# Kernel optimization log

Measured on AMD Instinct MI355X. Metric: run time of the kernel, lower is better.

The kernel has to match this reference:

```python
import jax, jax.numpy as jnp
import numpy as np

DIM_MODEL = 1024
NUM_HEADS = 16
DIM_HEAD = 64
B, S = 2, 2048


def setup_inputs() -> dict:
    key = jax.random.key(0)
    ks = jax.random.split(key, 10)
    scale = 1.0 / np.sqrt(DIM_MODEL)
    inp = {
        "x": jax.random.normal(ks[0], (B, S, DIM_MODEL), dtype=jnp.float32),
        "padding_mask": jax.random.randint(ks[1], (B, S), 0, 2, dtype=jnp.int32),
        "Wq": jax.random.normal(ks[2], (DIM_MODEL, DIM_MODEL), dtype=jnp.float32) * scale,
        "bq": jnp.zeros((DIM_MODEL,), dtype=jnp.float32),
        "Wk": jax.random.normal(ks[3], (DIM_MODEL, DIM_MODEL), dtype=jnp.float32) * scale,
        "bk": jnp.zeros((DIM_MODEL,), dtype=jnp.float32),
        "Wv": jax.random.normal(ks[4], (DIM_MODEL, DIM_MODEL), dtype=jnp.float32) * scale,
        "bv": jnp.zeros((DIM_MODEL,), dtype=jnp.float32),
        "Wo": jax.random.normal(ks[5], (DIM_MODEL, DIM_MODEL), dtype=jnp.float32) * scale,
        "bo": jnp.zeros((DIM_MODEL,), dtype=jnp.float32),
    }
    return inp


def reference(x, padding_mask, Wq, bq, Wk, bk, Wv, bv, Wo, bo):
    b, s, _ = x.shape
    dot_scale = jnp.sqrt(jnp.asarray(DIM_HEAD, dtype=x.dtype))
    # projections -> (b, h, s, d)
    q = (x @ Wq + bq).reshape(b, s, NUM_HEADS, DIM_HEAD).transpose(0, 2, 1, 3)
    k = (x @ Wk + bk).reshape(b, s, NUM_HEADS, DIM_HEAD).transpose(0, 2, 1, 3)
    v = (x @ Wv + bv).reshape(b, s, NUM_HEADS, DIM_HEAD).transpose(0, 2, 1, 3)
    # scores (b, h, s, s)
    scores = jnp.einsum("bhqd,bhkd->bhqk", q, k) / dot_scale
    mask = (padding_mask == 1)[:, None, None, :]  # (b,1,1,s) over key positions
    scores = jnp.where(mask, -jnp.inf, scores)
    attn = jax.nn.softmax(scores, axis=-1)
    out = jnp.einsum("bhqk,bhkd->bhqd", attn, v)
    out = out.transpose(0, 2, 1, 3).reshape(b, s, NUM_HEADS * DIM_HEAD)
    return out @ Wo + bo
```

## Files before the change

kernel.cpp:

```cpp
#include <hip/hip_runtime.h>
#include <hip/hip_bf16.h>
#include <stdint.h>
#include <math.h>

#define D_MODEL 1024
#define NHEAD   16
#define DHEAD   64
#define BATCH   2
#define SEQ     2048
#define M_TOK   (BATCH * SEQ)

#define QSCALE 0.18033688011112042f

typedef __attribute__((ext_vector_type(8))) short   short8;
typedef __attribute__((ext_vector_type(8))) __bf16  bf16x8;
typedef __attribute__((ext_vector_type(4))) float   f32x4;

__device__ inline short f2bf(float f) {
  unsigned int u = __builtin_bit_cast(unsigned int, f);
  unsigned int r = (u + 0x7FFFu + ((u >> 16) & 1u)) >> 16;
  return (short)(unsigned short)r;
}
__device__ inline short f2bf_fast(float f) {
  unsigned int u = __builtin_bit_cast(unsigned int, f);
  return (short)(unsigned short)((u + 0x8000u) >> 16);
}

__device__ inline void gl_lds16(const void* g, void* l) {
  __builtin_amdgcn_global_load_lds((__attribute__((address_space(1))) void*)(g),
                                   (__attribute__((address_space(3))) void*)(l),
                                   16, 0, 0);
}

__device__ inline bf16x8 lds_frag(const short* p) {
  return *(const bf16x8*)(p);
}

__global__ __launch_bounds__(256) void prep(const float* __restrict__ x,
                                            short* __restrict__ xb,
                                            const float* __restrict__ w0,
                                            const float* __restrict__ w1,
                                            const float* __restrict__ w2,
                                            const float* __restrict__ w3,
                                            short* __restrict__ out) {
  const int t = threadIdx.x;
  if (blockIdx.z == 4) {
    size_t base = ((size_t)blockIdx.y * 16 + blockIdx.x) * 16384;
    const float* in = x + base;
    short* o = xb + base;
#pragma unroll
    for (int i = 0; i < 16; ++i) {
      f32x4 v = *(const f32x4*)(in + (size_t)t * 4 + i * 1024);
      short4 s4;
      s4.x = f2bf(v[0]); s4.y = f2bf(v[1]); s4.z = f2bf(v[2]); s4.w = f2bf(v[3]);
      *(short4*)(o + (size_t)t * 4 + i * 1024) = s4;
    }
    return;
  }
  __shared__ short tile[64][72];
  const float* W = blockIdx.z == 0 ? w0 : blockIdx.z == 1 ? w1 : blockIdx.z == 2 ? w2 : w3;
  short* O = out + (size_t)blockIdx.z * (D_MODEL * (size_t)D_MODEL);
  int n0 = blockIdx.x * 64, k0 = blockIdx.y * 64;
#pragma unroll
  for (int i = 0; i < 16; ++i) {
    int idx = t + 256 * i;
    int r = idx >> 6, c = idx & 63;
    tile[r][c] = f2bf(W[(size_t)(k0 + r) * D_MODEL + n0 + c]);
  }
  __syncthreads();
#pragma unroll
  for (int i = 0; i < 16; ++i) {
    int idx = t + 256 * i;
    int r = idx >> 6, c = idx & 63;
    O[(size_t)(n0 + r) * D_MODEL + k0 + c] = tile[c][r];
  }
}

template <bool OUTF32, bool VT, int TN>
__global__ __launch_bounds__(256) void gemm128(const short* __restrict__ A,
                                               const short* __restrict__ Bt_base,
                                               const float* __restrict__ b0,
                                               const float* __restrict__ b1,
                                               const float* __restrict__ b2,
                                               void* __restrict__ out_base,
                                               short* __restrict__ vt,
                                               const int* __restrict__ pm) {
  constexpr int NI = TN / 32;
  const int z = blockIdx.z;
  const short* Bt   = Bt_base + (size_t)z * (D_MODEL * (size_t)D_MODEL);
  const float* bias = (z == 0) ? b0 : (z == 1) ? b1 : b2;

  __shared__ short As[128 * 64];
  __shared__ short Bs[TN * 64];

  const int t = threadIdx.x;
  const int lane = t & 63;
  const int wid = t >> 6;
  const int wm = (wid >> 1) * 64, wn = (wid & 1) * (TN / 2);
  const int m0 = blockIdx.x * 128, n0 = blockIdx.y * TN;
  const int cl = lane & 15, q = lane >> 4;
  const int sw = cl & 7;

  f32x4 acc[4][NI];
#pragma unroll
  for (int i = 0; i < 4; ++i)
#pragma unroll
    for (int j = 0; j < NI; ++j) acc[i][j] = 0.0f;

  for (int k0 = 0; k0 < D_MODEL; k0 += 64) {
    __syncthreads();
#pragma unroll
    for (int i = 0; i < 4; ++i) {
      int c = t + 256 * i;
      int row = c >> 3, cp = c & 7;
      int col = ((cp ^ (row & 7)) * 8);
      gl_lds16(A + (size_t)(m0 + row) * D_MODEL + k0 + col, (void*)(As + c * 8));
    }
#pragma unroll
    for (int i = 0; i < NI; ++i) {
      int c = t + 256 * i;
      int row = c >> 3, cp = c & 7;
      int col = ((cp ^ (row & 7)) * 8);
      gl_lds16(Bt + (size_t)(n0 + row) * D_MODEL + k0 + col, (void*)(Bs + c * 8));
    }
    __syncthreads();

    bf16x8 af[4][2], bfr[NI][2];
#pragma unroll
    for (int mi = 0; mi < 4; ++mi) {
      af[mi][0] = lds_frag(As + (wm + mi * 16 + cl) * 64 + (q ^ sw) * 8);
      af[mi][1] = lds_frag(As + (wm + mi * 16 + cl) * 64 + ((4 + q) ^ sw) * 8);
    }
#pragma unroll
    for (int ni = 0; ni < NI; ++ni) {
      bfr[ni][0] = lds_frag(Bs + (wn + ni * 16 + cl) * 64 + (q ^ sw) * 8);
      bfr[ni][1] = lds_frag(Bs + (wn + ni * 16 + cl) * 64 + ((4 + q) ^ sw) * 8);
    }
#pragma unroll
    for (int mi = 0; mi < 4; ++mi)
#pragma unroll
      for (int ni = 0; ni < NI; ++ni) {
        acc[mi][ni] = __builtin_amdgcn_mfma_f32_16x16x32_bf16(af[mi][0], bfr[ni][0], acc[mi][ni], 0, 0, 0);
        acc[mi][ni] = __builtin_amdgcn_mfma_f32_16x16x32_bf16(af[mi][1], bfr[ni][1], acc[mi][ni], 0, 0, 0);
      }
  }

  const float oscale = (VT && z == 0) ? QSCALE : 1.0f;
  int4 mm[4];
  if (VT && z == 2) {
#pragma unroll
    for (int mi = 0; mi < 4; ++mi) {
      int rbase = m0 + wm + mi * 16 + q * 4;
      mm[mi] = *(const int4*)(pm + (size_t)(rbase >> 11) * SEQ + (rbase & (SEQ - 1)));
    }
  }
#pragma unroll
  for (int ni = 0; ni < NI; ++ni) {
    int col = n0 + wn + ni * 16 + cl;
    float bv = bias[col];
#pragma unroll
    for (int mi = 0; mi < 4; ++mi) {
      int rbase = m0 + wm + mi * 16 + q * 4;
      if (VT && z == 2) {
        short4 o4;
        o4.x = (mm[mi].x == 1) ? (short)0 : f2bf_fast(acc[mi][ni][0] + bv);
        o4.y = (mm[mi].y == 1) ? (short)0 : f2bf_fast(acc[mi][ni][1] + bv);
        o4.z = (mm[mi].z == 1) ? (short)0 : f2bf_fast(acc[mi][ni][2] + bv);
        o4.w = (mm[mi].w == 1) ? (short)0 : f2bf_fast(acc[mi][ni][3] + bv);
        int btok = rbase >> 11;
        int s    = rbase & (SEQ - 1);
        int sp = (s & ~31) | ((s & 16) >> 2) | ((s & 12) << 1) | (s & 3);
        *(short4*)(vt + (size_t)btok * ((size_t)D_MODEL * SEQ) + (size_t)col * SEQ + sp) = o4;
      } else {
#pragma unroll
        for (int r = 0; r < 4; ++r) {
          float v = (acc[mi][ni][r] + bv) * oscale;
          size_t idx = (size_t)(rbase + r) * D_MODEL + col;
          if (OUTF32) {
            ((float*)out_base)[idx] = v;
          } else {
            short* out = (short*)out_base + (size_t)z * ((size_t)M_TOK * D_MODEL);
            out[idx] = f2bf_fast(v);
          }
        }
      }
    }
  }
}

__global__ __launch_bounds__(512) void attn_flash(const short* __restrict__ Q,
                                                  const short* __restrict__ K,
                                                  const short* __restrict__ Vt,
                                                  const int*   __restrict__ mask,
                                                  short* __restrict__ ctx) {
  const int qb = blockIdx.x;
  const int h  = blockIdx.y;
  const int b  = blockIdx.z;

  __shared__ __align__(16) short smem[28672];
  short* Qs  = smem;
  short* Ks  = smem + 8192;
  short* Vts = smem + 16384;
  float* Usf = (float*)(smem + 24576);

  const int t = threadIdx.x;
  const int lane = t & 63;
  const int wid = t >> 6;
  const int wg  = wid >> 1;
  const int kvh = wid & 1;
  const int cl = lane & 15, q = lane >> 4;
  const int sw = cl & 7;

  const size_t rowQ0 = (size_t)b * SEQ + (size_t)qb * 128;
  const size_t rowK0 = (size_t)b * SEQ;
  const size_t vbase = ((size_t)b * D_MODEL + h * DHEAD) * SEQ;

  const int srow = t >> 3, scp = t & 7;
  const int scol = (scp ^ (srow & 7)) * 8;
  const short* Kg0 = K + (rowK0 + srow) * D_MODEL + h * DHEAD + scol;
  const short* Kg1 = K + (rowK0 + 1024 + srow) * D_MODEL + h * DHEAD + scol;
  const short* Vg0 = Vt + vbase + (size_t)srow * SEQ + scol;
  const short* Vg1 = Vt + vbase + (size_t)srow * SEQ + 1024 + scol;

  short8 gk0 = *(const short8*)(Kg0);
  short8 gk1 = *(const short8*)(Kg1);
  short8 gv0 = *(const short8*)(Vg0);
  short8 gv1 = *(const short8*)(Vg1);

  {
    int4 mv = *(const int4*)(mask + (size_t)b * SEQ + t * 4);
    f32x4 u4;
    u4[0] = (mv.x == 1) ? 0.0f : 1.0f;
    u4[1] = (mv.y == 1) ? 0.0f : 1.0f;
    u4[2] = (mv.z == 1) ? 0.0f : 1.0f;
    u4[3] = (mv.w == 1) ? 0.0f : 1.0f;
    *(f32x4*)(Usf + t * 4) = u4;
  }

#pragma unroll
  for (int i = 0; i < 2; ++i) {
    int c = t + 512 * i;
    int row = c >> 3, cp = c & 7;
    gl_lds16(Q + (rowQ0 + row) * D_MODEL + h * DHEAD + ((cp ^ (row & 7)) * 8),
             (void*)(Qs + c * 8));
  }
  __syncthreads();

  bf16x8 qf[2][2];
#pragma unroll
  for (int rb = 0; rb < 2; ++rb) {
    int row = wg * 32 + rb * 16 + cl;
    qf[rb][0] = lds_frag(Qs + row * 64 + (q ^ sw) * 8);
    qf[rb][1] = lds_frag(Qs + row * 64 + ((4 + q) ^ sw) * 8);
  }
  const short* Kp = Ks  + kvh * 4096;
  const short* Vp = Vts + kvh * 4096;
  const float* Up = Usf + kvh * 1024;

  f32x4 lacc[2], oacc[2][4];
#pragma unroll
  for (int rb = 0; rb < 2; ++rb) {
    lacc[rb] = 0.0f;
#pragma unroll
    for (int dj = 0; dj < 4; ++dj) oacc[rb][dj] = 0.0f;
  }

  for (int s0 = 0; s0 < 1024; s0 += 64) {
    __syncthreads();

    *(short8*)(Ks  + t * 8)        = gk0;
    *(short8*)(Ks  + 4096 + t * 8) = gk1;
    *(short8*)(Vts + t * 8)        = gv0;
    *(short8*)(Vts + 4096 + t * 8) = gv1;
    __syncthreads();

    if (s0 + 64 < 1024) {
      int sn = s0 + 64;
      gk0 = *(const short8*)(Kg0 + (size_t)sn * D_MODEL);
      gk1 = *(const short8*)(Kg1 + (size_t)sn * D_MODEL);
      gv0 = *(const short8*)(Vg0 + sn);
      gv1 = *(const short8*)(Vg1 + sn);
    }

    f32x4 s[2][4];
#pragma unroll
    for (int j = 0; j < 4; ++j) {
      bf16x8 kf0 = lds_frag(Kp + (j * 16 + cl) * 64 + (q ^ sw) * 8);
      bf16x8 kf1 = lds_frag(Kp + (j * 16 + cl) * 64 + ((4 + q) ^ sw) * 8);
#pragma unroll
      for (int rb = 0; rb < 2; ++rb) {
        f32x4 sa = 0.0f;
        sa = __builtin_amdgcn_mfma_f32_16x16x32_bf16(kf0, qf[rb][0], sa, 0, 0, 0);
        sa = __builtin_amdgcn_mfma_f32_16x16x32_bf16(kf1, qf[rb][1], sa, 0, 0, 0);
        s[rb][j] = sa;
      }
    }

    f32x4 uv[4];
#pragma unroll
    for (int j = 0; j < 4; ++j)
      uv[j] = *(const f32x4*)(Up + s0 + j * 16 + 4 * q);
#pragma unroll
    for (int rb = 0; rb < 2; ++rb)
#pragma unroll
      for (int j = 0; j < 4; ++j) {
#pragma unroll
        for (int r = 0; r < 4; ++r)
          s[rb][j][r] = __builtin_amdgcn_exp2f(s[rb][j][r]) * uv[j][r];
        lacc[rb] += s[rb][j];
      }

    bf16x8 pf[2][2];
#pragma unroll
    for (int rb = 0; rb < 2; ++rb)
#pragma unroll
      for (int c = 0; c < 2; ++c) {
        bf16x8 v;
        v[0] = (__bf16)s[rb][2 * c][0];
        v[1] = (__bf16)s[rb][2 * c][1];
        v[2] = (__bf16)s[rb][2 * c][2];
        v[3] = (__bf16)s[rb][2 * c][3];
        v[4] = (__bf16)s[rb][2 * c + 1][0];
        v[5] = (__bf16)s[rb][2 * c + 1][1];
        v[6] = (__bf16)s[rb][2 * c + 1][2];
        v[7] = (__bf16)s[rb][2 * c + 1][3];
        pf[rb][c] = v;
      }

#pragma unroll
    for (int dj = 0; dj < 4; ++dj) {
      const short* vrow = Vp + (dj * 16 + cl) * 64;
#pragma unroll
      for (int c = 0; c < 2; ++c) {
        bf16x8 vfc = lds_frag(vrow + (((4 * c + q) ^ sw) * 8));
#pragma unroll
        for (int rb = 0; rb < 2; ++rb)
          oacc[rb][dj] = __builtin_amdgcn_mfma_f32_16x16x32_bf16(vfc, pf[rb][c], oacc[rb][dj], 0, 0, 0);
      }
    }
  }

  __syncthreads();
  float hl[2];
#pragma unroll
  for (int rb = 0; rb < 2; ++rb)
    hl[rb] = lacc[rb][0] + lacc[rb][1] + lacc[rb][2] + lacc[rb][3];

  float* redO = (float*)smem;
  float* redL = (float*)(smem + 16384);
  const int slot = wg * 64 + lane;
  if (kvh) {
#pragma unroll
    for (int rb = 0; rb < 2; ++rb) {
#pragma unroll
      for (int dj = 0; dj < 4; ++dj) {
        int qi = (rb * 4 + dj) ^ (lane & 7);
        *(f32x4*)(redO + slot * 32 + qi * 4) = oacc[rb][dj];
      }
      redL[slot * 2 + rb] = hl[rb];
    }
  }
  __syncthreads();
  if (kvh) return;
#pragma unroll
  for (int rb = 0; rb < 2; ++rb) {
    hl[rb] += redL[slot * 2 + rb];
#pragma unroll
    for (int dj = 0; dj < 4; ++dj) {
      int qi = (rb * 4 + dj) ^ (lane & 7);
      oacc[rb][dj] += *(const f32x4*)(redO + slot * 32 + qi * 4);
    }
  }
#pragma unroll
  for (int rb = 0; rb < 2; ++rb) {
    hl[rb] += __shfl_xor(hl[rb], 16);
    hl[rb] += __shfl_xor(hl[rb], 32);
  }

#pragma unroll
  for (int rb = 0; rb < 2; ++rb) {
    float inv = (hl[rb] > 0.0f) ? 1.0f / hl[rb] : 0.0f;
    size_t row = rowQ0 + wg * 32 + rb * 16 + cl;
#pragma unroll
    for (int dj = 0; dj < 4; ++dj) {
      short4 o4;
      o4.x = f2bf(oacc[rb][dj][0] * inv);
      o4.y = f2bf(oacc[rb][dj][1] * inv);
      o4.z = f2bf(oacc[rb][dj][2] * inv);
      o4.w = f2bf(oacc[rb][dj][3] * inv);
      *(short4*)(ctx + row * D_MODEL + h * DHEAD + dj * 16 + q * 4) = o4;
    }
  }
}

extern "C" void kernel_launch(void* const* d_in, const int* in_sizes, int n_in,
                              void* d_out, int out_size, void* d_ws, size_t ws_size,
                              hipStream_t stream) {
  (void)in_sizes; (void)n_in; (void)out_size; (void)ws_size;

  const float* x  = (const float*)d_in[0];
  const int*   pm = (const int*)  d_in[1];
  const float* Wq = (const float*)d_in[2];
  const float* bq = (const float*)d_in[3];
  const float* Wk = (const float*)d_in[4];
  const float* bk = (const float*)d_in[5];
  const float* Wv = (const float*)d_in[6];
  const float* bv = (const float*)d_in[7];
  const float* Wo = (const float*)d_in[8];
  const float* bo = (const float*)d_in[9];

  const size_t WMAT = (size_t)D_MODEL * D_MODEL;
  const size_t TOKD = (size_t)M_TOK * D_MODEL;

  short* base = (short*)d_ws;
  short* Wt = base;
  short* xb = base + 4 * WMAT;
  short* Qw = xb + TOKD;
  short* Kw = Qw + TOKD;
  short* Vtw = Kw + TOKD;
  short* Cw = Vtw + TOKD;

  prep<<<dim3(16, 16, 5), 256, 0, stream>>>(x, xb, Wq, Wk, Wv, Wo, Wt);
  gemm128<false, true, 128><<<dim3(M_TOK / 128, D_MODEL / 128, 3), 256, 0, stream>>>(
      xb, Wt, bq, bk, bv, Qw, Vtw, pm);
  attn_flash<<<dim3(SEQ / 128, NHEAD, BATCH), 512, 0, stream>>>(Qw, Kw, Vtw, pm, Cw);
  gemm128<true, false, 64><<<dim3(M_TOK / 128, D_MODEL / 64, 1), 256, 0, stream>>>(
      Cw, Wt + 3 * WMAT, bo, bo, bo, d_out, nullptr, nullptr);
}
```

Baseline: 207.0 us.

## Double-buffer K/V tiles in LDS with direct global-to-LDS loads and additive mask

Replaces the register-staged K/V prefetch with two LDS buffers filled by direct global-to-LDS copies, alternating stage and compute so the next tile's load overlaps the current tile's MFMA work. The key-padding mask becomes an additive bias (-1e30) that seeds the MFMA accumulator, which removes the per-element multiply after exp2. LDS use grows and the loop is unrolled by two, which may lower occupancy. The asynchronous LDS writes must be complete before the barrier for correctness.

```diff
diff --git a/kernel.cpp b/kernel.cpp
--- a/kernel.cpp
+++ b/kernel.cpp
@@ -197,11 +197,10 @@
   const int h  = blockIdx.y;
   const int b  = blockIdx.z;
 
-  __shared__ __align__(16) short smem[28672];
-  short* Qs  = smem;
-  short* Ks  = smem + 8192;
-  short* Vts = smem + 16384;
-  float* Usf = (float*)(smem + 24576);
+  __shared__ __align__(16) short smem[36864];
+  short* bufA = smem;
+  short* bufB = smem + 16384;
+  float* Usf  = (float*)(smem + 32768);
 
   const int t = threadIdx.x;
   const int lane = t & 63;
@@ -222,27 +221,29 @@
   const short* Vg0 = Vt + vbase + (size_t)srow * SEQ + scol;
   const short* Vg1 = Vt + vbase + (size_t)srow * SEQ + 1024 + scol;
 
-  short8 gk0 = *(const short8*)(Kg0);
-  short8 gk1 = *(const short8*)(Kg1);
-  short8 gv0 = *(const short8*)(Vg0);
-  short8 gv1 = *(const short8*)(Vg1);
-
-  {
-    int4 mv = *(const int4*)(mask + (size_t)b * SEQ + t * 4);
-    f32x4 u4;
-    u4[0] = (mv.x == 1) ? 0.0f : 1.0f;
-    u4[1] = (mv.y == 1) ? 0.0f : 1.0f;
-    u4[2] = (mv.z == 1) ? 0.0f : 1.0f;
-    u4[3] = (mv.w == 1) ? 0.0f : 1.0f;
-    *(f32x4*)(Usf + t * 4) = u4;
-  }
-
+  auto stage = [&](short* buf, int sn) {
+    gl_lds16(Kg0 + (size_t)sn * D_MODEL, (void*)(buf + t * 8));
+    gl_lds16(Kg1 + (size_t)sn * D_MODEL, (void*)(buf + 4096 + t * 8));
+    gl_lds16(Vg0 + sn,                   (void*)(buf + 8192 + t * 8));
+    gl_lds16(Vg1 + sn,                   (void*)(buf + 8192 + 4096 + t * 8));
+  };
+
+  stage(bufA, 0);
 #pragma unroll
   for (int i = 0; i < 2; ++i) {
     int c = t + 512 * i;
     int row = c >> 3, cp = c & 7;
     gl_lds16(Q + (rowQ0 + row) * D_MODEL + h * DHEAD + ((cp ^ (row & 7)) * 8),
-             (void*)(Qs + c * 8));
+             (void*)(bufB + c * 8));
+  }
+  {
+    int4 mv = *(const int4*)(mask + (size_t)b * SEQ + t * 4);
+    f32x4 u4;
+    u4[0] = (mv.x == 1) ? -1e30f : 0.0f;
+    u4[1] = (mv.y == 1) ? -1e30f : 0.0f;
+    u4[2] = (mv.z == 1) ? -1e30f : 0.0f;
+    u4[3] = (mv.w == 1) ? -1e30f : 0.0f;
+    *(f32x4*)(Usf + t * 4) = u4;
   }
   __syncthreads();
 
@@ -250,12 +251,9 @@
 #pragma unroll
   for (int rb = 0; rb < 2; ++rb) {
     int row = wg * 32 + rb * 16 + cl;
-    qf[rb][0] = lds_frag(Qs + row * 64 + (q ^ sw) * 8);
-    qf[rb][1] = lds_frag(Qs + row * 64 + ((4 + q) ^ sw) * 8);
-  }
-  const short* Kp = Ks  + kvh * 4096;
-  const short* Vp = Vts + kvh * 4096;
-  const float* Up = Usf + kvh * 1024;
+    qf[rb][0] = lds_frag(bufB + row * 64 + (q ^ sw) * 8);
+    qf[rb][1] = lds_frag(bufB + row * 64 + ((4 + q) ^ sw) * 8);
+  }
 
   f32x4 lacc[2], oacc[2][4];
 #pragma unroll
@@ -265,48 +263,33 @@
     for (int dj = 0; dj < 4; ++dj) oacc[rb][dj] = 0.0f;
   }
 
-  for (int s0 = 0; s0 < 1024; s0 += 64) {
-    __syncthreads();
-
-    *(short8*)(Ks  + t * 8)        = gk0;
-    *(short8*)(Ks  + 4096 + t * 8) = gk1;
-    *(short8*)(Vts + t * 8)        = gv0;
-    *(short8*)(Vts + 4096 + t * 8) = gv1;
-    __syncthreads();
-
-    if (s0 + 64 < 1024) {
-      int sn = s0 + 64;
-      gk0 = *(const short8*)(Kg0 + (size_t)sn * D_MODEL);
-      gk1 = *(const short8*)(Kg1 + (size_t)sn * D_MODEL);
-      gv0 = *(const short8*)(Vg0 + sn);
-      gv1 = *(const short8*)(Vg1 + sn);
-    }
+  auto compute = [&](const short* buf, int s0) {
+    const short* Kp = buf + kvh * 4096;
+    const short* Vp = buf + 8192 + kvh * 4096;
+    const float* Bp = Usf + kvh * 1024 + s0 + 4 * q;
 
     f32x4 s[2][4];
 #pragma unroll
     for (int j = 0; j < 4; ++j) {
       bf16x8 kf0 = lds_frag(Kp + (j * 16 + cl) * 64 + (q ^ sw) * 8);
       bf16x8 kf1 = lds_frag(Kp + (j * 16 + cl) * 64 + ((4 + q) ^ sw) * 8);
+      f32x4 cv = *(const f32x4*)(Bp + j * 16);
 #pragma unroll
       for (int rb = 0; rb < 2; ++rb) {
-        f32x4 sa = 0.0f;
+        f32x4 sa = cv;
         sa = __builtin_amdgcn_mfma_f32_16x16x32_bf16(kf0, qf[rb][0], sa, 0, 0, 0);
         sa = __builtin_amdgcn_mfma_f32_16x16x32_bf16(kf1, qf[rb][1], sa, 0, 0, 0);
         s[rb][j] = sa;
       }
     }
 
-    f32x4 uv[4];
-#pragma unroll
-    for (int j = 0; j < 4; ++j)
-      uv[j] = *(const f32x4*)(Up + s0 + j * 16 + 4 * q);
 #pragma unroll
     for (int rb = 0; rb < 2; ++rb)
 #pragma unroll
       for (int j = 0; j < 4; ++j) {
 #pragma unroll
         for (int r = 0; r < 4; ++r)
-          s[rb][j][r] = __builtin_amdgcn_exp2f(s[rb][j][r]) * uv[j][r];
+          s[rb][j][r] = __builtin_amdgcn_exp2f(s[rb][j][r]);
         lacc[rb] += s[rb][j];
       }
 
@@ -338,6 +321,16 @@
           oacc[rb][dj] = __builtin_amdgcn_mfma_f32_16x16x32_bf16(vfc, pf[rb][c], oacc[rb][dj], 0, 0, 0);
       }
     }
+  };
+
+  for (int it = 0; it < 8; ++it) {
+    int s0 = it * 128;
+    __syncthreads();
+    stage(bufB, s0 + 64);
+    compute(bufA, s0);
+    __syncthreads();
+    if (it < 7) stage(bufA, s0 + 128);
+    compute(bufB, s0 + 64);
   }
 
   __syncthreads();
```

After: 192.7 us. 1.07x faster.
